# Performance work log

Measured on AMD Instinct MI355X. Metric: run time of the kernel, lower is better.

The kernel has to match this reference:

```python
import jax, jax.numpy as jnp
import numpy as np

N_HEADS = 16
HEAD_DIM = 64
ROPE_THETA = 10000.0


def rotate_half(x):
    x1, x2 = jnp.split(x, 2, axis=-1)
    return jnp.concatenate([-x2, x1], axis=-1)


def setup_inputs() -> dict:
    key = jax.random.key(0)
    k0, k1, k2 = jax.random.split(key, 3)
    B, L, C = 2, 2048, 1024
    x = jax.random.normal(k0, (B, L, C), dtype=jnp.float32)
    # causal additive bias, as used by VAR-style blockwise masks (here full causal)
    causal = jnp.tril(jnp.ones((L, L), dtype=bool))
    attn_bias = jnp.where(causal, 0.0, -1e9).astype(jnp.float32)[None, None]
    position_ids = jnp.broadcast_to(jnp.arange(L, dtype=jnp.int32), (B, L))
    qkv_w = 0.02 * jax.random.normal(k1, (3 * C, C), dtype=jnp.float32)
    q_bias = jnp.zeros((C,), jnp.float32)
    v_bias = jnp.zeros((C,), jnp.float32)
    proj_w = 0.02 * jax.random.normal(k2, (C, C), dtype=jnp.float32)
    proj_b = jnp.zeros((C,), jnp.float32)
    return {"x": x, "attn_bias": attn_bias, "position_ids": position_ids,
            "qkv_w": qkv_w, "q_bias": q_bias, "v_bias": v_bias,
            "proj_w": proj_w, "proj_b": proj_b}


def reference(x, attn_bias, position_ids, qkv_w, q_bias, v_bias, proj_w, proj_b):
    B, L, C = x.shape
    H, D = N_HEADS, HEAD_DIM
    # fused QKV projection with concatenated (q_bias, 0, v_bias)
    bias = jnp.concatenate([q_bias, jnp.zeros_like(q_bias), v_bias])
    qkv = (jnp.einsum('blc,oc->blo', x, qkv_w) + bias).reshape(B, L, 3, H, D)
    q = jnp.transpose(qkv[:, :, 0], (0, 2, 1, 3))  # [B,H,L,D]
    k = jnp.transpose(qkv[:, :, 1], (0, 2, 1, 3))
    v = jnp.transpose(qkv[:, :, 2], (0, 2, 1, 3))
    # Llama rotary embedding: cos/sin [B,L,D] -> unsqueeze dim=1
    inv_freq = 1.0 / (ROPE_THETA ** (jnp.arange(0, D, 2, dtype=jnp.float32) / D))
    freqs = position_ids.astype(jnp.float32)[:, :, None] * inv_freq  # [B,L,D/2]
    emb = jnp.concatenate([freqs, freqs], axis=-1)
    cos = jnp.cos(emb)[:, None]  # [B,1,L,D]
    sin = jnp.sin(emb)[:, None]
    q = q * cos + rotate_half(q) * sin
    k = k * cos + rotate_half(k) * sin
    # slow_attn: (q*scale) @ k^T + bias -> softmax -> @ v
    scale = 0.25 / np.sqrt(D).astype(np.float32)
    attn = jnp.einsum('bhqd,bhkd->bhqk', q * scale, k) + attn_bias
    attn = jax.nn.softmax(attn, axis=-1)
    out = jnp.einsum('bhqk,bhkd->bhqd', attn, v)
    out = out.transpose(0, 2, 1, 3).reshape(B, L, C)
    return jnp.einsum('blc,oc->blo', out, proj_w) + proj_b
```

## Files before the change

### kernel.cpp

```cpp
#include <hip/hip_runtime.h>

typedef unsigned short u16;
typedef unsigned int u32;
typedef __attribute__((ext_vector_type(8))) short short8;
typedef __attribute__((ext_vector_type(4))) float f32x4;
typedef __attribute__((ext_vector_type(2))) unsigned int u32x2;
typedef __attribute__((ext_vector_type(4))) unsigned short u16x4;
typedef __attribute__((ext_vector_type(8))) unsigned short u16x8;

#define AS1 __attribute__((address_space(1)))
#define AS3 __attribute__((address_space(3)))

__device__ __forceinline__ u16 f2bf(float f) {
  u32 u = __builtin_bit_cast(u32, f);
  u32 r = u + 0x7FFFu + ((u >> 16) & 1u);
  return (u16)(r >> 16);
}
__device__ __forceinline__ float bf2f(u16 h) {
  u32 u = ((u32)h) << 16;
  return __builtin_bit_cast(float, u);
}
__device__ __forceinline__ void gload_lds16(const void* g, void* l) {
  __builtin_amdgcn_global_load_lds((AS1 void*)g, (AS3 void*)l, 16, 0, 0);
}

#define QSCALE 0.04508422002778011f

__device__ __forceinline__ void cvt_body(const float* __restrict__ src, u16* __restrict__ dst,
                                         int i) {
  float4 v = ((const float4*)src)[i];
  u16x4 o;
  o[0] = f2bf(v.x); o[1] = f2bf(v.y); o[2] = f2bf(v.z); o[3] = f2bf(v.w);
  ((u16x4*)dst)[i] = o;
}

__global__ __launch_bounds__(256)
void pre_kernel(const float* __restrict__ x, const float* __restrict__ w1,
                const float* __restrict__ w2, const int* __restrict__ pos,
                u16* __restrict__ x_bf, u16* __restrict__ w1_bf, u16* __restrict__ w2_bf,
                float* __restrict__ tab) {
  int bid = blockIdx.x;
  int t = threadIdx.x;
  if (bid < 4096) {
    cvt_body(x, x_bf, bid * 256 + t);
  } else if (bid < 7168) {
    cvt_body(w1, w1_bf, (bid - 4096) * 256 + t);
  } else if (bid < 8192) {
    cvt_body(w2, w2_bf, (bid - 7168) * 256 + t);
  } else {
    int idx = (bid - 8192) * 256 + t;
    int i = idx & 31;
    int bl = idx >> 5;
    float p = (float)pos[bl];
    float inv_freq = 1.0f / powf(10000.0f, (2.0f * (float)i) / 64.0f);
    float ang = p * inv_freq;
    tab[(size_t)bl * 64 + i] = cosf(ang);
    tab[(size_t)bl * 64 + 32 + i] = sinf(ang);
  }
}

template <bool OUT_BF16>
__global__ __launch_bounds__(256)
void gemm_bt_kernel(const u16* __restrict__ A, const u16* __restrict__ Bw,
                    void* __restrict__ Cout, const float* __restrict__ bias,
                    int M, int N, int K, int NXT) {
  __shared__ alignas(16) u16 As[128 * 64];
  __shared__ alignas(16) u16 Bs[128 * 64];
  const int tid = threadIdx.x;
  const int lane = tid & 63, wave = tid >> 6;
  const int wr = wave >> 1, wc = wave & 1;
  const int nblk = gridDim.x;
  const int lin = (blockIdx.x & 7) * (nblk >> 3) + (blockIdx.x >> 3);
  const int m0 = (lin / NXT) * 128, n0 = (lin % NXT) * 128;
  const int r = lane & 15, g = lane >> 4;

  f32x4 acc[4][4] = {};

  const int nk = K >> 6;
  for (int kt = 0; kt < nk; ++kt) {
    const int k0 = kt << 6;
#pragma unroll
    for (int c = 0; c < 4; ++c) {
      int i = c * 256 + tid;
      int row = i >> 3, slot = i & 7;
      int ss = slot ^ (row & 7);
      const u16* gA = A + (size_t)(m0 + row) * K + k0 + ss * 8;
      const u16* gB = Bw + (size_t)(n0 + row) * K + k0 + ss * 8;
      void* lA = (char*)As + c * 4096 + wave * 1024;
      void* lB = (char*)Bs + c * 4096 + wave * 1024;
      gload_lds16(gA, lA);
      gload_lds16(gB, lB);
    }
    __syncthreads();
#pragma unroll
    for (int kk = 0; kk < 2; ++kk) {
      short8 af[4], bf[4];
#pragma unroll
      for (int m = 0; m < 4; ++m) {
        int row = wr * 64 + m * 16 + r;
        int byte = row * 128 + (((kk * 4 + g) ^ (row & 7)) << 4);
        af[m] = *(const short8*)((const char*)As + byte);
      }
#pragma unroll
      for (int n = 0; n < 4; ++n) {
        int row = wc * 64 + n * 16 + r;
        int byte = row * 128 + (((kk * 4 + g) ^ (row & 7)) << 4);
        bf[n] = *(const short8*)((const char*)Bs + byte);
      }
#pragma unroll
      for (int m = 0; m < 4; ++m)
#pragma unroll
        for (int n = 0; n < 4; ++n)
          acc[m][n] = __builtin_amdgcn_mfma_f32_16x16x32_bf16(af[m], bf[n], acc[m][n], 0, 0, 0);
    }
    __syncthreads();
  }

  if constexpr (OUT_BF16) {
    u16* C = (u16*)Cout;
#pragma unroll
    for (int m = 0; m < 4; ++m) {
      int rg = m0 + wr * 64 + m * 16 + g * 4;
#pragma unroll
      for (int n = 0; n < 4; ++n) {
        int cg = n0 + wc * 64 + n * 16 + r;
#pragma unroll
        for (int j = 0; j < 4; ++j)
          C[(size_t)(rg + j) * N + cg] = f2bf(acc[m][n][j]);
      }
    }
  } else {
    float* C = (float*)Cout;
#pragma unroll
    for (int m = 0; m < 4; ++m) {
      int rg = m0 + wr * 64 + m * 16 + g * 4;
#pragma unroll
      for (int n = 0; n < 4; ++n) {
        int cg = n0 + wc * 64 + n * 16 + r;
        float bv = bias[cg];
#pragma unroll
        for (int j = 0; j < 4; ++j)
          C[(size_t)(rg + j) * N + cg] = acc[m][n][j] + bv;
      }
    }
  }
}

__global__ __launch_bounds__(256)
void gemm_bt64_kernel(const u16* __restrict__ A, const u16* __restrict__ Bw,
                      float* __restrict__ Cout, const float* __restrict__ bias,
                      int M, int N, int K, int NXT) {
  __shared__ alignas(16) u16 As[128 * 64];
  __shared__ alignas(16) u16 Bs[64 * 64];
  const int tid = threadIdx.x;
  const int lane = tid & 63, wave = tid >> 6;
  const int wr = wave >> 1, wc = wave & 1;
  const int nblk = gridDim.x;
  const int lin = (blockIdx.x & 7) * (nblk >> 3) + (blockIdx.x >> 3);
  const int m0 = (lin / NXT) * 128, n0 = (lin % NXT) * 64;
  const int r = lane & 15, g = lane >> 4;

  f32x4 acc[4][2] = {};

  const int nk = K >> 6;
  for (int kt = 0; kt < nk; ++kt) {
    const int k0 = kt << 6;
#pragma unroll
    for (int c = 0; c < 4; ++c) {
      int i = c * 256 + tid;
      int row = i >> 3, slot = i & 7;
      int ss = slot ^ (row & 7);
      const u16* gA = A + (size_t)(m0 + row) * K + k0 + ss * 8;
      void* lA = (char*)As + c * 4096 + wave * 1024;
      gload_lds16(gA, lA);
    }
#pragma unroll
    for (int c = 0; c < 2; ++c) {
      int i = c * 256 + tid;
      int row = i >> 3, slot = i & 7;
      int ss = slot ^ (row & 7);
      const u16* gB = Bw + (size_t)(n0 + row) * K + k0 + ss * 8;
      void* lB = (char*)Bs + c * 4096 + wave * 1024;
      gload_lds16(gB, lB);
    }
    __syncthreads();
#pragma unroll
    for (int kk = 0; kk < 2; ++kk) {
      short8 af[4], bf[2];
#pragma unroll
      for (int m = 0; m < 4; ++m) {
        int row = wr * 64 + m * 16 + r;
        int byte = row * 128 + (((kk * 4 + g) ^ (row & 7)) << 4);
        af[m] = *(const short8*)((const char*)As + byte);
      }
#pragma unroll
      for (int n = 0; n < 2; ++n) {
        int row = wc * 32 + n * 16 + r;
        int byte = row * 128 + (((kk * 4 + g) ^ (row & 7)) << 4);
        bf[n] = *(const short8*)((const char*)Bs + byte);
      }
#pragma unroll
      for (int m = 0; m < 4; ++m)
#pragma unroll
        for (int n = 0; n < 2; ++n)
          acc[m][n] = __builtin_amdgcn_mfma_f32_16x16x32_bf16(af[m], bf[n], acc[m][n], 0, 0, 0);
    }
    __syncthreads();
  }

#pragma unroll
  for (int m = 0; m < 4; ++m) {
    int rg = m0 + wr * 64 + m * 16 + g * 4;
#pragma unroll
    for (int n = 0; n < 2; ++n) {
      int cg = n0 + wc * 32 + n * 16 + r;
      float bv = bias[cg];
#pragma unroll
      for (int j = 0; j < 4; ++j)
        Cout[(size_t)(rg + j) * N + cg] = acc[m][n][j] + bv;
    }
  }
}

__global__ __launch_bounds__(256)
void mid_kernel(const u16* __restrict__ qkv, const float* __restrict__ tab,
                const float* __restrict__ q_bias, const float* __restrict__ v_bias,
                u16* __restrict__ Qo, u16* __restrict__ Ko, u16* __restrict__ vt) {
  __shared__ alignas(16) u16 tile[64][72];
  int bid = blockIdx.x;
  int t = threadIdx.x;
  if (bid < 4096) {
    int bl = bid;
    int b = bl >> 11, l = bl & 2047;
    const float* tr = tab + (size_t)bl * 64;
    const u16* base = qkv + (size_t)bl * 3072;
#pragma unroll
    for (int pp = 0; pp < 2; ++pp) {
      int p = t + pp * 256;
      int h = p >> 5, d = p & 31;
      float c = tr[d], s = tr[32 + d];
      size_t o = ((size_t)(b * 16 + h) * 2048 + l) * 64 + d;
      float x1 = bf2f(base[h * 64 + d]) + q_bias[h * 64 + d];
      float x2 = bf2f(base[h * 64 + d + 32]) + q_bias[h * 64 + d + 32];
      Qo[o]      = f2bf((x1 * c - x2 * s) * QSCALE);
      Qo[o + 32] = f2bf((x2 * c + x1 * s) * QSCALE);
      x1 = bf2f(base[1024 + h * 64 + d]);
      x2 = bf2f(base[1024 + h * 64 + d + 32]);
      Ko[o]      = f2bf(x1 * c - x2 * s);
      Ko[o + 32] = f2bf(x2 * c + x1 * s);
    }
  } else {
    int bid2 = bid - 4096;
    int bh = bid2 >> 5;
    int b = bh >> 4, h = bh & 15;
    int l0 = (bid2 & 31) * 64;
    int rr = t >> 2;
    int c0 = (t & 3) * 16;
    const u16* src = qkv + ((size_t)(b * 2048 + l0 + rr)) * 3072 + 2048 + h * 64 + c0;
    u16x8 a = *(const u16x8*)src;
    u16x8 bb = *(const u16x8*)(src + 8);
#pragma unroll
    for (int i = 0; i < 8; ++i) {
      a[i]  = f2bf(bf2f(a[i])  + v_bias[h * 64 + c0 + i]);
      bb[i] = f2bf(bf2f(bb[i]) + v_bias[h * 64 + c0 + 8 + i]);
    }
    *(u16x8*)&tile[rr][c0] = a;
    *(u16x8*)&tile[rr][c0 + 8] = bb;
    __syncthreads();
    int d = t >> 2;
    int lc = (t & 3) * 16;
    u16x8 o1, o2;
#pragma unroll
    for (int i = 0; i < 8; ++i) {
      o1[i] = tile[lc + i][d];
      o2[i] = tile[lc + 8 + i][d];
    }
    u16* dst = vt + ((size_t)bh * 64 + d) * 2048 + l0 + lc;
    *(u16x8*)dst = o1;
    *(u16x8*)(dst + 8) = o2;
  }
}

__global__ __launch_bounds__(512)
void attn_kernel(const u16* __restrict__ Q, const u16* __restrict__ Kmat,
                 const u16* __restrict__ Vt, u16* __restrict__ O) {
  __shared__ alignas(16) u16 Ks[3][64 * 64];
  __shared__ alignas(16) u16 Vs[3][64 * 64];
  __shared__ alignas(16) u16 Pbuf[8][1024];
  const int tid = threadIdx.x;
  const int lane = tid & 63;
  const int wave = tid >> 6;
  const int id = blockIdx.x;
  const int xcd = id & 7, rank = id >> 3;
  const int bh = xcd + 8 * (rank & 3);
  const int xqA = 31 - (rank >> 2);
  const int wt = wave >> 2;
  const int xq = wt ? (xqA - 16) : xqA;
  const int ntA = xqA + 1;
  const int nt = xq + 1;
  const int b = bh >> 4, h = bh & 15;
  const int r = lane & 15, g = lane >> 4;

  const u16* Kb = Kmat + (size_t)bh * 2048 * 64;
  const u16* Vb = Vt + (size_t)bh * 64 * 2048;

  const int srow = wave * 8 + (lane >> 3);
  const int sslot = (lane & 7) ^ (srow & 7);

#define STAGE(tt, bb) do { \
    gload_lds16(Kb + ((size_t)((tt) * 64 + srow)) * 64 + sslot * 8, \
                (char*)Ks[bb] + wave * 1024); \
    gload_lds16(Vb + (size_t)srow * 2048 + (tt) * 64 + sslot * 8, \
                (char*)Vs[bb] + wave * 1024); \
  } while (0)

  u16* Pw = Pbuf[wave];
  const int qrow0 = xq * 64 + (wave & 3) * 16;
  const u16* Qb = Q + ((size_t)bh * 2048 + qrow0) * 64;

  short8 qf[2];
#pragma unroll
  for (int kk = 0; kk < 2; ++kk)
    qf[kk] = *(const short8*)(Qb + r * 64 + kk * 32 + g * 8);

  f32x4 o_acc[4] = {};
  float l_run = 0.f;

  STAGE(0, 0);
  STAGE(1, 1);
  asm volatile("s_waitcnt vmcnt(2)" ::: "memory");
  __builtin_amdgcn_s_barrier();

  for (int t = 0; t < ntA; ++t) {
    if (t + 2 < ntA) STAGE(t + 2, (t + 2) % 3);

    if (t < nt) {
      const char* Kc = (const char*)Ks[t % 3];
      const char* Vc = (const char*)Vs[t % 3];
      const int kv0 = t * 64;

      f32x4 s[4] = {};
      __builtin_amdgcn_s_setprio(1);
#pragma unroll
      for (int ct = 0; ct < 4; ++ct) {
#pragma unroll
        for (int kk = 0; kk < 2; ++kk) {
          int row = ct * 16 + r;
          int byte = row * 128 + (((kk * 4 + g) ^ (row & 7)) << 4);
          short8 kf = *(const short8*)(Kc + byte);
          s[ct] = __builtin_amdgcn_mfma_f32_16x16x32_bf16(kf, qf[kk], s[ct], 0, 0, 0);
        }
      }
      __builtin_amdgcn_s_setprio(0);

      if (kv0 + 63 > qrow0) {
        int qrow = qrow0 + r;
#pragma unroll
        for (int ct = 0; ct < 4; ++ct)
#pragma unroll
          for (int j = 0; j < 4; ++j) {
            int kv = kv0 + ct * 16 + 4 * g + j;
            if (kv > qrow) s[ct][j] = -1e30f;
          }
      }

      u32x2 pk[4];
#pragma unroll
      for (int ct = 0; ct < 4; ++ct) {
        float p0 = exp2f(s[ct][0]);
        float p1 = exp2f(s[ct][1]);
        float p2 = exp2f(s[ct][2]);
        float p3 = exp2f(s[ct][3]);
        l_run += (p0 + p1) + (p2 + p3);
        u32 lo, hi;
        asm("v_cvt_pk_bf16_f32 %0, %1, %2" : "=v"(lo) : "v"(p0), "v"(p1));
        asm("v_cvt_pk_bf16_f32 %0, %1, %2" : "=v"(hi) : "v"(p2), "v"(p3));
        pk[ct][0] = lo;
        pk[ct][1] = hi;
      }

#pragma unroll
      for (int ct = 0; ct < 4; ++ct) {
        int byte = r * 128 + ((32 * ct + 8 * g) ^ ((r & 7) << 4));
        *(u32x2*)((char*)Pw + byte) = pk[ct];
      }

      __builtin_amdgcn_s_setprio(1);
#pragma unroll
      for (int kk = 0; kk < 2; ++kk) {
        int byte = r * 128 + (((kk * 4 + g) ^ (r & 7)) << 4);
        short8 pf = *(const short8*)((const char*)Pw + byte);
#pragma unroll
        for (int n = 0; n < 4; ++n) {
          int row = n * 16 + r;
          int vbyte = row * 128 + (((kk * 4 + g) ^ (row & 7)) << 4);
          short8 vf = *(const short8*)(Vc + vbyte);
          o_acc[n] = __builtin_amdgcn_mfma_f32_16x16x32_bf16(pf, vf, o_acc[n], 0, 0, 0);
        }
      }
      __builtin_amdgcn_s_setprio(0);
    }

    if (t + 1 < ntA) {
      if (t + 2 < ntA) {
        asm volatile("s_waitcnt vmcnt(2)" ::: "memory");
      } else {
        asm volatile("s_waitcnt vmcnt(0)" ::: "memory");
      }
      __builtin_amdgcn_s_barrier();
    }
  }
#undef STAGE

  l_run += __shfl_xor(l_run, 16, 64);
  l_run += __shfl_xor(l_run, 32, 64);
  float linv = 1.0f / l_run;
  float ij[4];
#pragma unroll
  for (int j = 0; j < 4; ++j) ij[j] = __shfl(linv, 4 * g + j, 64);
#pragma unroll
  for (int n = 0; n < 4; ++n)
#pragma unroll
    for (int j = 0; j < 4; ++j) {
      size_t idx = ((size_t)b * 2048 + qrow0 + 4 * g + j) * 1024 + h * 64 + n * 16 + r;
      O[idx] = f2bf(o_acc[n][j] * ij[j]);
    }
}

extern "C" void kernel_launch(void* const* d_in, const int* in_sizes, int n_in,
                              void* d_out, int out_size, void* d_ws, size_t ws_size,
                              hipStream_t stream) {
  const float* x      = (const float*)d_in[0];
  const int*   pos    = (const int*)d_in[2];
  const float* qkv_w  = (const float*)d_in[3];
  const float* q_bias = (const float*)d_in[4];
  const float* v_bias = (const float*)d_in[5];
  const float* proj_w = (const float*)d_in[6];
  const float* proj_b = (const float*)d_in[7];
  float* out = (float*)d_out;

  char* ws = (char*)d_ws;
  u16* x_bf    = (u16*)(ws + 0);
  u16* w1_bf   = (u16*)(ws + 8388608);
  u16* w2_bf   = (u16*)(ws + 14680064);
  u16* qkv_bf  = (u16*)(ws + 16777216);
  u16* q_bf    = (u16*)(ws + 41943040);
  u16* k_bf    = (u16*)(ws + 50331648);
  u16* vt_bf   = (u16*)(ws + 58720256);
  u16* attn_bf = (u16*)(ws + 67108864);
  float* tab   = (float*)(ws + 75497472);

  pre_kernel<<<8704, 256, 0, stream>>>(x, qkv_w, proj_w, pos, x_bf, w1_bf, w2_bf, tab);
  gemm_bt_kernel<true><<<768, 256, 0, stream>>>(x_bf, w1_bf, qkv_bf, nullptr,
                                                4096, 3072, 1024, 24);
  mid_kernel<<<5120, 256, 0, stream>>>(qkv_bf, tab, q_bias, v_bias, q_bf, k_bf, vt_bf);
  attn_kernel<<<512, 512, 0, stream>>>(q_bf, k_bf, vt_bf, attn_bf);
  gemm_bt64_kernel<<<512, 256, 0, stream>>>(attn_bf, w2_bf, out, proj_b,
                                            4096, 1024, 1024, 16);
}
```

Baseline: 118.6 us.

## Restructure attention blocks to 4 waves each owning 32 query rows

The attention kernel now runs 256-thread blocks of 4 waves. Each wave handles two 16-row query halves, so K and V fragments loaded from LDS are reused across both halves. Each block covers a contiguous 128-row query tile, and work is balanced by pairing long and short tiles across blocks, replacing the earlier scheme that paired two 64-row tiles per block. This cuts LDS read traffic per MFMA and per-block staging overhead, at the cost of more registers per wave and fewer waves per CU.

```diff
diff --git a/kernel.cpp b/kernel.cpp
--- a/kernel.cpp
+++ b/kernel.cpp
@@ -281,129 +281,146 @@
   }
 }
 
-__global__ __launch_bounds__(512)
+__global__ __launch_bounds__(256)
 void attn_kernel(const u16* __restrict__ Q, const u16* __restrict__ Kmat,
                  const u16* __restrict__ Vt, u16* __restrict__ O) {
   __shared__ alignas(16) u16 Ks[3][64 * 64];
   __shared__ alignas(16) u16 Vs[3][64 * 64];
-  __shared__ alignas(16) u16 Pbuf[8][1024];
+  __shared__ alignas(16) u16 Pbuf[4][2048];
   const int tid = threadIdx.x;
   const int lane = tid & 63;
   const int wave = tid >> 6;
   const int id = blockIdx.x;
   const int xcd = id & 7, rank = id >> 3;
-  const int bh = xcd + 8 * (rank & 3);
-  const int xqA = 31 - (rank >> 2);
-  const int wt = wave >> 2;
-  const int xq = wt ? (xqA - 16) : xqA;
-  const int ntA = xqA + 1;
-  const int nt = xq + 1;
+  const int grp = rank >> 4;
+  const int w = rank & 15;
+  const int bh = xcd + 8 * grp;
+  const int qx = (w & 1) ? (w >> 1) : (15 - (w >> 1));
+  const int nt = 2 * qx + 2;
   const int b = bh >> 4, h = bh & 15;
   const int r = lane & 15, g = lane >> 4;
 
   const u16* Kb = Kmat + (size_t)bh * 2048 * 64;
   const u16* Vb = Vt + (size_t)bh * 64 * 2048;
 
-  const int srow = wave * 8 + (lane >> 3);
-  const int sslot = (lane & 7) ^ (srow & 7);
+  const int srow0 = tid >> 3;
+  const int sslot0 = (tid & 7) ^ (srow0 & 7);
+  const int srow1 = srow0 + 32;
+  const int sslot1 = (tid & 7) ^ (srow1 & 7);
 
 #define STAGE(tt, bb) do { \
-    gload_lds16(Kb + ((size_t)((tt) * 64 + srow)) * 64 + sslot * 8, \
+    gload_lds16(Kb + ((size_t)((tt) * 64 + srow0)) * 64 + sslot0 * 8, \
                 (char*)Ks[bb] + wave * 1024); \
-    gload_lds16(Vb + (size_t)srow * 2048 + (tt) * 64 + sslot * 8, \
+    gload_lds16(Kb + ((size_t)((tt) * 64 + srow1)) * 64 + sslot1 * 8, \
+                (char*)Ks[bb] + 4096 + wave * 1024); \
+    gload_lds16(Vb + (size_t)srow0 * 2048 + (tt) * 64 + sslot0 * 8, \
                 (char*)Vs[bb] + wave * 1024); \
+    gload_lds16(Vb + (size_t)srow1 * 2048 + (tt) * 64 + sslot1 * 8, \
+                (char*)Vs[bb] + 4096 + wave * 1024); \
   } while (0)
 
   u16* Pw = Pbuf[wave];
-  const int qrow0 = xq * 64 + (wave & 3) * 16;
+  const int qrow0 = qx * 128 + wave * 32;
   const u16* Qb = Q + ((size_t)bh * 2048 + qrow0) * 64;
 
-  short8 qf[2];
-#pragma unroll
-  for (int kk = 0; kk < 2; ++kk)
-    qf[kk] = *(const short8*)(Qb + r * 64 + kk * 32 + g * 8);
-
-  f32x4 o_acc[4] = {};
-  float l_run = 0.f;
+  short8 qf[2][2];
+#pragma unroll
+  for (int qh = 0; qh < 2; ++qh)
+#pragma unroll
+    for (int kk = 0; kk < 2; ++kk)
+      qf[qh][kk] = *(const short8*)(Qb + (qh * 16 + r) * 64 + kk * 32 + g * 8);
+
+  f32x4 o_acc[2][4] = {};
+  float l_run[2] = {0.f, 0.f};
 
   STAGE(0, 0);
   STAGE(1, 1);
-  asm volatile("s_waitcnt vmcnt(2)" ::: "memory");
+  asm volatile("s_waitcnt vmcnt(4)" ::: "memory");
   __builtin_amdgcn_s_barrier();
 
-  for (int t = 0; t < ntA; ++t) {
-    if (t + 2 < ntA) STAGE(t + 2, (t + 2) % 3);
-
-    if (t < nt) {
-      const char* Kc = (const char*)Ks[t % 3];
-      const char* Vc = (const char*)Vs[t % 3];
-      const int kv0 = t * 64;
-
-      f32x4 s[4] = {};
-      __builtin_amdgcn_s_setprio(1);
-#pragma unroll
-      for (int ct = 0; ct < 4; ++ct) {
-#pragma unroll
-        for (int kk = 0; kk < 2; ++kk) {
-          int row = ct * 16 + r;
-          int byte = row * 128 + (((kk * 4 + g) ^ (row & 7)) << 4);
-          short8 kf = *(const short8*)(Kc + byte);
-          s[ct] = __builtin_amdgcn_mfma_f32_16x16x32_bf16(kf, qf[kk], s[ct], 0, 0, 0);
-        }
-      }
-      __builtin_amdgcn_s_setprio(0);
-
-      if (kv0 + 63 > qrow0) {
-        int qrow = qrow0 + r;
+  for (int t = 0; t < nt; ++t) {
+    if (t + 2 < nt) STAGE(t + 2, (t + 2) % 3);
+
+    const char* Kc = (const char*)Ks[t % 3];
+    const char* Vc = (const char*)Vs[t % 3];
+    const int kv0 = t * 64;
+
+    short8 kf[4][2];
+#pragma unroll
+    for (int ct = 0; ct < 4; ++ct)
+#pragma unroll
+      for (int kk = 0; kk < 2; ++kk) {
+        int row = ct * 16 + r;
+        kf[ct][kk] = *(const short8*)(Kc + row * 128 + (((kk * 4 + g) ^ (row & 7)) << 4));
+      }
+
+    f32x4 s[2][4] = {};
+    __builtin_amdgcn_s_setprio(1);
+#pragma unroll
+    for (int qh = 0; qh < 2; ++qh)
+#pragma unroll
+      for (int ct = 0; ct < 4; ++ct)
+#pragma unroll
+        for (int kk = 0; kk < 2; ++kk)
+          s[qh][ct] = __builtin_amdgcn_mfma_f32_16x16x32_bf16(kf[ct][kk], qf[qh][kk],
+                                                             s[qh][ct], 0, 0, 0);
+    __builtin_amdgcn_s_setprio(0);
+
+    if (kv0 + 63 > qrow0) {
+#pragma unroll
+      for (int qh = 0; qh < 2; ++qh) {
+        int qrow = qrow0 + qh * 16 + r;
 #pragma unroll
         for (int ct = 0; ct < 4; ++ct)
 #pragma unroll
           for (int j = 0; j < 4; ++j) {
             int kv = kv0 + ct * 16 + 4 * g + j;
-            if (kv > qrow) s[ct][j] = -1e30f;
+            if (kv > qrow) s[qh][ct][j] = -1e30f;
           }
       }
-
-      u32x2 pk[4];
+    }
+
+#pragma unroll
+    for (int qh = 0; qh < 2; ++qh) {
 #pragma unroll
       for (int ct = 0; ct < 4; ++ct) {
-        float p0 = exp2f(s[ct][0]);
-        float p1 = exp2f(s[ct][1]);
-        float p2 = exp2f(s[ct][2]);
-        float p3 = exp2f(s[ct][3]);
-        l_run += (p0 + p1) + (p2 + p3);
-        u32 lo, hi;
-        asm("v_cvt_pk_bf16_f32 %0, %1, %2" : "=v"(lo) : "v"(p0), "v"(p1));
-        asm("v_cvt_pk_bf16_f32 %0, %1, %2" : "=v"(hi) : "v"(p2), "v"(p3));
-        pk[ct][0] = lo;
-        pk[ct][1] = hi;
-      }
-
-#pragma unroll
-      for (int ct = 0; ct < 4; ++ct) {
-        int byte = r * 128 + ((32 * ct + 8 * g) ^ ((r & 7) << 4));
-        *(u32x2*)((char*)Pw + byte) = pk[ct];
-      }
-
-      __builtin_amdgcn_s_setprio(1);
-#pragma unroll
-      for (int kk = 0; kk < 2; ++kk) {
-        int byte = r * 128 + (((kk * 4 + g) ^ (r & 7)) << 4);
+        float p0 = exp2f(s[qh][ct][0]);
+        float p1 = exp2f(s[qh][ct][1]);
+        float p2 = exp2f(s[qh][ct][2]);
+        float p3 = exp2f(s[qh][ct][3]);
+        l_run[qh] += (p0 + p1) + (p2 + p3);
+        u32x2 pk;
+        asm("v_cvt_pk_bf16_f32 %0, %1, %2" : "=v"(pk[0]) : "v"(p0), "v"(p1));
+        asm("v_cvt_pk_bf16_f32 %0, %1, %2" : "=v"(pk[1]) : "v"(p2), "v"(p3));
+        int byte = (qh * 16 + r) * 128 + ((32 * ct + 8 * g) ^ ((r & 7) << 4));
+        *(u32x2*)((char*)Pw + byte) = pk;
+      }
+    }
+
+    __builtin_amdgcn_s_setprio(1);
+#pragma unroll
+    for (int kk = 0; kk < 2; ++kk) {
+      short8 vf[4];
+#pragma unroll
+      for (int n = 0; n < 4; ++n) {
+        int row = n * 16 + r;
+        vf[n] = *(const short8*)(Vc + row * 128 + (((kk * 4 + g) ^ (row & 7)) << 4));
+      }
+#pragma unroll
+      for (int qh = 0; qh < 2; ++qh) {
+        int byte = (qh * 16 + r) * 128 + (((kk * 4 + g) ^ (r & 7)) << 4);
         short8 pf = *(const short8*)((const char*)Pw + byte);
 #pragma unroll
-        for (int n = 0; n < 4; ++n) {
-          int row = n * 16 + r;
-          int vbyte = row * 128 + (((kk * 4 + g) ^ (row & 7)) << 4);
-          short8 vf = *(const short8*)(Vc + vbyte);
-          o_acc[n] = __builtin_amdgcn_mfma_f32_16x16x32_bf16(pf, vf, o_acc[n], 0, 0, 0);
-        }
-      }
-      __builtin_amdgcn_s_setprio(0);
-    }
-
-    if (t + 1 < ntA) {
-      if (t + 2 < ntA) {
-        asm volatile("s_waitcnt vmcnt(2)" ::: "memory");
+        for (int n = 0; n < 4; ++n)
+          o_acc[qh][n] = __builtin_amdgcn_mfma_f32_16x16x32_bf16(pf, vf[n],
+                                                                o_acc[qh][n], 0, 0, 0);
+      }
+    }
+    __builtin_amdgcn_s_setprio(0);
+
+    if (t + 1 < nt) {
+      if (t + 2 < nt) {
+        asm volatile("s_waitcnt vmcnt(4)" ::: "memory");
       } else {
         asm volatile("s_waitcnt vmcnt(0)" ::: "memory");
       }
@@ -412,19 +429,24 @@
   }
 #undef STAGE
 
-  l_run += __shfl_xor(l_run, 16, 64);
-  l_run += __shfl_xor(l_run, 32, 64);
-  float linv = 1.0f / l_run;
-  float ij[4];
-#pragma unroll
-  for (int j = 0; j < 4; ++j) ij[j] = __shfl(linv, 4 * g + j, 64);
-#pragma unroll
-  for (int n = 0; n < 4; ++n)
-#pragma unroll
-    for (int j = 0; j < 4; ++j) {
-      size_t idx = ((size_t)b * 2048 + qrow0 + 4 * g + j) * 1024 + h * 64 + n * 16 + r;
-      O[idx] = f2bf(o_acc[n][j] * ij[j]);
-    }
+#pragma unroll
+  for (int qh = 0; qh < 2; ++qh) {
+    float lr = l_run[qh];
+    lr += __shfl_xor(lr, 16, 64);
+    lr += __shfl_xor(lr, 32, 64);
+    float linv = 1.0f / lr;
+    float ij[4];
+#pragma unroll
+    for (int j = 0; j < 4; ++j) ij[j] = __shfl(linv, 4 * g + j, 64);
+#pragma unroll
+    for (int n = 0; n < 4; ++n)
+#pragma unroll
+      for (int j = 0; j < 4; ++j) {
+        size_t idx = ((size_t)b * 2048 + qrow0 + qh * 16 + 4 * g + j) * 1024
+                     + h * 64 + n * 16 + r;
+        O[idx] = f2bf(o_acc[qh][n][j] * ij[j]);
+      }
+  }
 }
 
 extern "C" void kernel_launch(void* const* d_in, const int* in_sizes, int n_in,
@@ -454,7 +476,7 @@
   gemm_bt_kernel<true><<<768, 256, 0, stream>>>(x_bf, w1_bf, qkv_bf, nullptr,
                                                 4096, 3072, 1024, 24);
   mid_kernel<<<5120, 256, 0, stream>>>(qkv_bf, tab, q_bias, v_bias, q_bf, k_bf, vt_bf);
-  attn_kernel<<<512, 512, 0, stream>>>(q_bf, k_bf, vt_bf, attn_bf);
+  attn_kernel<<<512, 256, 0, stream>>>(q_bf, k_bf, vt_bf, attn_bf);
   gemm_bt64_kernel<<<512, 256, 0, stream>>>(attn_bf, w2_bf, out, proj_b,
                                             4096, 1024, 1024, 16);
 }
```

Measured after the change: 145.8 us. 23.0% more time.
